# Kernel tuning notes

Measured on AMD Instinct MI355X. Metric: run time of the kernel, lower is better.

The kernel has to match this reference:

```python
import jax, jax.numpy as jnp
import numpy as np


def setup_inputs() -> dict:
    key = jax.random.key(0)
    k1, k2, k3, k4, k5 = jax.random.split(key, 5)
    b, c, k, h, w = 8, 512, 19, 128, 128
    x = jax.random.normal(k1, (b, c, h, w), dtype=jnp.float32)
    # mask_conv: 1x1 conv ichn->ochn (weight [k, c], bias [k])
    Wm = jax.random.normal(k2, (k, c), dtype=jnp.float32) * (1.0 / np.sqrt(c))
    bm = jax.random.normal(k3, (k,), dtype=jnp.float32) * 0.02
    # filter_conv: grouped 1x1 conv, groups=k -> per-class [c_out, c_in] matmul
    Wf = jax.random.normal(k4, (k, c, c), dtype=jnp.float32) * (1.0 / np.sqrt(c))
    bf = jax.random.normal(k5, (k, c), dtype=jnp.float32) * 0.02
    return {"x": x, "Wm": Wm, "bm": bm, "Wf": Wf, "bf": bf}


def reference(x, Wm, bm, Wf, bf):
    b, c, h, w = x.shape
    k = Wm.shape[0]
    # mask_conv (1x1) + sigmoid -> [b, k, h, w]
    pre_mask = jnp.einsum('bchw,kc->bkhw', x, Wm) + bm[None, :, None, None]
    mask = jax.nn.sigmoid(pre_mask)
    # masked pooling: bmm(mask [b,k,hw], feat [b,hw,c]) / (h*w) -> [b, k, c]
    class_feat = jnp.einsum('bkhw,bchw->bkc', mask, x) / (h * w)
    # grouped 1x1 filter_conv: per class k, [c_out, c_in] GEMM on class_feat
    filters = jnp.einsum('koc,bkc->bko', Wf, class_feat) + bf[None, :, :]  # [b, k, c]
    # per-sample dynamic 1x1 conv (groups=b) == batched GEMM over channels
    pred = jnp.einsum('bkc,bchw->bkhw', filters, x)
    return pred
```

## Files before the change

### kernel.cpp

```cpp
#include <hip/hip_runtime.h>
#include <math.h>

#define BB 8
#define CC 512
#define KK 19
#define HWHW 16384
#define INV_HW (1.0f/16384.0f)

typedef __attribute__((ext_vector_type(8))) short bf16x8;
typedef __attribute__((ext_vector_type(4))) short s16x4;
typedef __attribute__((ext_vector_type(4))) float f32x4;

__device__ __forceinline__ unsigned short f2bf(float f) {
    unsigned int u = __float_as_uint(f);
    u = (u + 0x7fffu + ((u >> 16) & 1u)) >> 16;
    return (unsigned short)u;
}

__device__ __forceinline__ unsigned int pk_bf16(float a, float b) {
    unsigned int r;
    asm("v_cvt_pk_bf16_f32 %0, %1, %2" : "=v"(r) : "v"(a), "v"(b));
    return r;
}

__global__ __launch_bounds__(256, 3) void k_s1(const float* __restrict__ x,
                                               const float* __restrict__ Wm,
                                               const float* __restrict__ bm,
                                               unsigned short* __restrict__ mask,
                                               unsigned short* __restrict__ xt4g,
                                               unsigned short* __restrict__ xt2g) {
    __shared__ short wm[20 * CC];
    __shared__ short xt[2][128 * 64];
    const int tid = threadIdx.x;
    const int b = blockIdx.x >> 7;
    const int pt = blockIdx.x & 127;
    const int p0 = pt << 7;
    const float* xb = x + ((size_t)b * CC) * HWHW + p0;

    for (int u = tid; u < 20 * 128; u += 256) {
        const int k = u >> 7;
        const int c4 = (u & 127) << 2;
        float4 w = {0.f, 0.f, 0.f, 0.f};
        if (k < KK) w = *(const float4*)(Wm + k * CC + c4);
        s16x4 v = { (short)f2bf(w.x), (short)f2bf(w.y), (short)f2bf(w.z), (short)f2bf(w.w) };
        *(s16x4*)&wm[(k << 9) + (((c4 >> 3) ^ (k & 7)) << 3) + (c4 & 7)] = v;
    }

    const int wv = tid >> 6, ln = tid & 63;
    const int lm = ln & 15, q = ln >> 4;
    const f32x4 zz = {0.f, 0.f, 0.f, 0.f};
    f32x4 acc[2][2];
    acc[0][0] = zz; acc[0][1] = zz; acc[1][0] = zz; acc[1][1] = zz;

    const int cg0 = tid >> 5;
    const int pA  = (tid & 31) << 2;
    const int pqT = (tid & 31) & 15;
    const int sS  = pt >> 3;
    const int kpT = ((pt & 7) << 1) | ((tid & 31) >> 4);
    const float* sA = xb + (size_t)(cg0 << 2) * HWHW + pA;
    const float* sB = xb + (size_t)((cg0 + 8) << 2) * HWHW + pA;
    unsigned short* t4fix = xt4g + ((size_t)((b << 7) | pt) << 16);
    unsigned short* t2fix = xt2g + ((size_t)(b << 3) << 20)
                                 + ((size_t)((sS << 4) | kpT) << 12);

    float4 Fa[8], Fb[8];
#pragma unroll
    for (int j = 0; j < 4; ++j) {
        Fa[j]     = *(const float4*)(sA + (size_t)j * HWHW);
        Fa[4 + j] = *(const float4*)(sB + (size_t)j * HWHW);
    }

#pragma unroll
    for (int cs = 0; cs < 8; ++cs) {
        const float4* cur = (cs & 1) ? Fb : Fa;
        float4* nxt = (cs & 1) ? Fa : Fb;
        if (cs < 7) {
            const size_t co = (size_t)((cs + 1) << 6) * HWHW;
#pragma unroll
            for (int j = 0; j < 4; ++j) {
                nxt[j]     = *(const float4*)(sA + co + (size_t)j * HWHW);
                nxt[4 + j] = *(const float4*)(sB + co + (size_t)j * HWHW);
            }
        }
        short* xts = (short*)xt[cs & 1];
        unsigned short* t4 = t4fix + ((size_t)cs << 13);
        unsigned short* t2 = t2fix + ((size_t)cs << 20);
#pragma unroll
        for (int h = 0; h < 2; ++h) {
            const int cg = cg0 + (h << 3);
            const float* G0 = (const float*)&cur[(h << 2) + 0];
            const float* G1 = (const float*)&cur[(h << 2) + 1];
            const float* G2 = (const float*)&cur[(h << 2) + 2];
            const float* G3 = (const float*)&cur[(h << 2) + 3];
#pragma unroll
            for (int j = 0; j < 4; ++j) {
                const int pr = pA + j;
                uint2 v = make_uint2(pk_bf16(G0[j], G1[j]), pk_bf16(G2[j], G3[j]));
                const int idx = (pr << 6) + (((cg >> 1) ^ (pr & 7)) << 3) + ((cg & 1) << 2);
                *(uint2*)&xts[idx] = v;
                *(uint2*)&t4[idx] = v;
            }
#pragma unroll
            for (int rr = 0; rr < 4; ++rr) {
                const int cl = (cg << 2) + rr;
                const float* Gr = (const float*)&cur[(h << 2) + rr];
                uint2 w = make_uint2(pk_bf16(Gr[0], Gr[1]), pk_bf16(Gr[2], Gr[3]));
                const int idx2 = (cl << 6) + (((pqT >> 1) ^ (cl & 7)) << 3) + ((pqT & 1) << 2);
                *(uint2*)&t2[idx2] = w;
            }
        }
        asm volatile("s_waitcnt lgkmcnt(0)" ::: "memory");
        __builtin_amdgcn_s_barrier();
        asm volatile("" ::: "memory");
#pragma unroll
        for (int ks = 0; ks < 2; ++ks) {
            const int gch = (cs << 3) + (ks << 2) + q;
            const int m1 = (lm < 3) ? (16 + lm) : 19;
            bf16x8 a0 = *(const bf16x8*)&wm[(lm << 9) + ((gch ^ (lm & 7)) << 3)];
            bf16x8 a1 = *(const bf16x8*)&wm[(m1 << 9) + ((gch ^ (m1 & 7)) << 3)];
            const int lch = (ks << 2) + q;
#pragma unroll
            for (int nt = 0; nt < 2; ++nt) {
                const int pr = (((wv << 1) + nt) << 4) + lm;
                bf16x8 bv = *(const bf16x8*)&xts[(pr << 6) + ((lch ^ (pr & 7)) << 3)];
                acc[0][nt] = __builtin_amdgcn_mfma_f32_16x16x32_bf16(a0, bv, acc[0][nt], 0, 0, 0);
                acc[1][nt] = __builtin_amdgcn_mfma_f32_16x16x32_bf16(a1, bv, acc[1][nt], 0, 0, 0);
            }
        }
    }

    unsigned short* mb = mask + ((size_t)b * KK) * HWHW + p0;
#pragma unroll
    for (int mt = 0; mt < 2; ++mt)
#pragma unroll
        for (int r = 0; r < 4; ++r) {
            const int k = (mt << 4) + (q << 2) + r;
            if (k < KK) {
                const float bias = bm[k];
#pragma unroll
                for (int nt = 0; nt < 2; ++nt) {
                    const int p = (((wv << 1) + nt) << 4) + lm;
                    const float t = acc[mt][nt][r] + bias;
                    mb[(size_t)k * HWHW + p] = f2bf(1.0f / (1.0f + __expf(-t)));
                }
            }
        }
}

__global__ __launch_bounds__(256, 4) void k_s2(const unsigned short* __restrict__ xt2g,
                                               const unsigned short* __restrict__ mask,
                                               float* __restrict__ cf_part) {
    __shared__ short mt_[2][20 * 64];
    __shared__ short xtl[2][64 * 64];
    const int tid = threadIdx.x;
    const int s = blockIdx.x & 15;
    const int ct = (blockIdx.x >> 4) & 7;
    const int b = blockIdx.x >> 7;
    const int wv = tid >> 6, ln = tid & 63;
    const int lm = ln & 15, q = ln >> 4;
    const unsigned short* mbs = mask + ((size_t)b * KK) * HWHW + (s << 10);
    const unsigned short* tb = xt2g + ((size_t)((((b << 3) | ct) << 4) | s) << 16);

    const int mk = tid >> 3, mch = tid & 7;

    const f32x4 zz = {0.f, 0.f, 0.f, 0.f};
    f32x4 acc[2];
    acc[0] = zz; acc[1] = zz;

    uint4 Xa[2], Xb2[2];
    uint4 Ma = make_uint4(0u,0u,0u,0u), Mb = make_uint4(0u,0u,0u,0u);

    if (tid < 160 && mk < KK) Ma = *(const uint4*)(mbs + (size_t)mk * HWHW + (mch << 3));
    Xa[0] = *(const uint4*)(tb + (tid << 4));
    Xa[1] = *(const uint4*)(tb + (tid << 4) + 8);

#pragma unroll
    for (int kp = 0; kp < 16; ++kp) {
        const uint4* curX = (kp & 1) ? Xb2 : Xa;
        uint4* nxtX = (kp & 1) ? Xa : Xb2;
        const uint4 curM = (kp & 1) ? Mb : Ma;
        uint4* nxtM = (kp & 1) ? &Ma : &Mb;
        if (kp < 15) {
            if (tid < 160 && mk < KK)
                *nxtM = *(const uint4*)(mbs + (size_t)mk * HWHW + ((kp + 1) << 6) + (mch << 3));
            nxtX[0] = *(const uint4*)(tb + ((kp + 1) << 12) + (tid << 4));
            nxtX[1] = *(const uint4*)(tb + ((kp + 1) << 12) + (tid << 4) + 8);
        }
        short* mts = (short*)mt_[kp & 1];
        short* xls = (short*)xtl[kp & 1];
        if (tid < 160)
            *(uint4*)&mts[(mk << 6) + ((mch ^ (mk & 7)) << 3)] = curM;
        *(uint4*)&xls[(tid << 4)] = curX[0];
        *(uint4*)&xls[(tid << 4) + 8] = curX[1];
        asm volatile("s_waitcnt lgkmcnt(0)" ::: "memory");
        __builtin_amdgcn_s_barrier();
        asm volatile("" ::: "memory");
#pragma unroll
        for (int ks = 0; ks < 2; ++ks) {
            const int pch = (ks << 2) + q;
            const int cr = (wv << 4) + lm;
            bf16x8 bv = *(const bf16x8*)&xls[(cr << 6) + ((pch ^ (cr & 7)) << 3)];
            const int m1 = (lm < 3) ? (16 + lm) : 19;
            bf16x8 a0 = *(const bf16x8*)&mts[(lm << 6) + ((pch ^ (lm & 7)) << 3)];
            bf16x8 a1 = *(const bf16x8*)&mts[(m1 << 6) + ((pch ^ (m1 & 7)) << 3)];
            acc[0] = __builtin_amdgcn_mfma_f32_16x16x32_bf16(a0, bv, acc[0], 0, 0, 0);
            acc[1] = __builtin_amdgcn_mfma_f32_16x16x32_bf16(a1, bv, acc[1], 0, 0, 0);
        }
    }

    float* dst = cf_part + ((size_t)(s * BB + b) * KK) * CC + (ct << 6) + (wv << 4) + lm;
#pragma unroll
    for (int mt = 0; mt < 2; ++mt)
#pragma unroll
        for (int r = 0; r < 4; ++r) {
            const int k = (mt << 4) + (q << 2) + r;
            if (k < KK) dst[(size_t)k * CC] = acc[mt][r];
        }
}

__global__ __launch_bounds__(256) void k_s2r(const float* __restrict__ part,
                                             float* __restrict__ cf) {
    const int i = blockIdx.x * 256 + threadIdx.x;
    if (i >= BB * KK * CC) return;
    const int b = i / (KK * CC);
    const int rem = i - b * (KK * CC);
    float sum = 0.0f;
#pragma unroll
    for (int s = 0; s < 16; ++s)
        sum += part[((size_t)(s * BB + b) * KK) * CC + rem];
    cf[i] = sum * INV_HW;
}

__global__ __launch_bounds__(256) void k_filters(const float* __restrict__ Wf,
                                                 const float* __restrict__ bf,
                                                 const float* __restrict__ cf,
                                                 float* __restrict__ fil) {
    const int blk = blockIdx.x;
    const int k = blk >> 7;
    const int o = ((blk & 127) << 2) + (threadIdx.x >> 6);
    const int lane = threadIdx.x & 63;
    const float* wrow = Wf + ((size_t)k * CC + o) * CC;

    float acc[BB];
#pragma unroll
    for (int b = 0; b < BB; ++b) acc[b] = 0.0f;
#pragma unroll
    for (int j = 0; j < CC / 64; ++j) {
        const int c = lane + (j << 6);
        const float wv = wrow[c];
#pragma unroll
        for (int b = 0; b < BB; ++b)
            acc[b] += wv * cf[((size_t)b * KK + k) * CC + c];
    }
#pragma unroll
    for (int b = 0; b < BB; ++b) {
#pragma unroll
        for (int off = 32; off > 0; off >>= 1)
            acc[b] += __shfl_down(acc[b], off, 64);
    }
    if (lane == 0) {
        const float bias = bf[k * CC + o];
#pragma unroll
        for (int b = 0; b < BB; ++b)
            fil[((size_t)b * KK + k) * CC + o] = acc[b] + bias;
    }
}

__global__ __launch_bounds__(256, 3) void k_s4(const unsigned short* __restrict__ xt4g,
                                               const float* __restrict__ fil,
                                               float* __restrict__ out) {
    __shared__ short wm[20 * CC];
    __shared__ short xt[2][128 * 64];
    const int tid = threadIdx.x;
    const int b = blockIdx.x >> 7;
    const int pt = blockIdx.x & 127;
    const int p0 = pt << 7;
    const float* fb = fil + ((size_t)b * KK) * CC;
    const unsigned short* tb = xt4g + ((size_t)((b << 7) | pt) << 16);

    for (int u = tid; u < 20 * 128; u += 256) {
        const int k = u >> 7;
        const int c4 = (u & 127) << 2;
        float4 w = {0.f, 0.f, 0.f, 0.f};
        if (k < KK) w = *(const float4*)(fb + k * CC + c4);
        s16x4 v = { (short)f2bf(w.x), (short)f2bf(w.y), (short)f2bf(w.z), (short)f2bf(w.w) };
        *(s16x4*)&wm[(k << 9) + (((c4 >> 3) ^ (k & 7)) << 3) + (c4 & 7)] = v;
    }

    const int wv = tid >> 6, ln = tid & 63;
    const int lm = ln & 15, q = ln >> 4;
    const f32x4 zz = {0.f, 0.f, 0.f, 0.f};
    f32x4 acc[2][2];
    acc[0][0] = zz; acc[0][1] = zz; acc[1][0] = zz; acc[1][1] = zz;

    uint4 Ta[4], Tb4[4];
#pragma unroll
    for (int r = 0; r < 4; ++r)
        Ta[r] = *(const uint4*)(tb + (tid << 5) + (r << 3));

#pragma unroll
    for (int cs = 0; cs < 8; ++cs) {
        const uint4* cur = (cs & 1) ? Tb4 : Ta;
        uint4* nxt = (cs & 1) ? Ta : Tb4;
        if (cs < 7) {
#pragma unroll
            for (int r = 0; r < 4; ++r)
                nxt[r] = *(const uint4*)(tb + ((cs + 1) << 13) + (tid << 5) + (r << 3));
        }
        short* xts = (short*)xt[cs & 1];
#pragma unroll
        for (int r = 0; r < 4; ++r)
            *(uint4*)&xts[(tid << 5) + (r << 3)] = cur[r];
        asm volatile("s_waitcnt lgkmcnt(0)" ::: "memory");
        __builtin_amdgcn_s_barrier();
        asm volatile("" ::: "memory");
#pragma unroll
        for (int ks = 0; ks < 2; ++ks) {
            const int gch = (cs << 3) + (ks << 2) + q;
            const int m1 = (lm < 3) ? (16 + lm) : 19;
            bf16x8 a0 = *(const bf16x8*)&wm[(lm << 9) + ((gch ^ (lm & 7)) << 3)];
            bf16x8 a1 = *(const bf16x8*)&wm[(m1 << 9) + ((gch ^ (m1 & 7)) << 3)];
            const int lch = (ks << 2) + q;
#pragma unroll
            for (int nt = 0; nt < 2; ++nt) {
                const int pr = (((wv << 1) + nt) << 4) + lm;
                bf16x8 bv = *(const bf16x8*)&xts[(pr << 6) + ((lch ^ (pr & 7)) << 3)];
                acc[0][nt] = __builtin_amdgcn_mfma_f32_16x16x32_bf16(a0, bv, acc[0][nt], 0, 0, 0);
                acc[1][nt] = __builtin_amdgcn_mfma_f32_16x16x32_bf16(a1, bv, acc[1][nt], 0, 0, 0);
            }
        }
    }

    float* ob = out + ((size_t)b * KK) * HWHW + p0;
#pragma unroll
    for (int mt = 0; mt < 2; ++mt)
#pragma unroll
        for (int r = 0; r < 4; ++r) {
            const int k = (mt << 4) + (q << 2) + r;
            if (k < KK) {
#pragma unroll
                for (int nt = 0; nt < 2; ++nt) {
                    const int p = (((wv << 1) + nt) << 4) + lm;
                    ob[(size_t)k * HWHW + p] = acc[mt][nt][r];
                }
            }
        }
}

extern "C" void kernel_launch(void* const* d_in, const int* in_sizes, int n_in,
                              void* d_out, int out_size, void* d_ws, size_t ws_size,
                              hipStream_t stream) {
    const float* x  = (const float*)d_in[0];
    const float* Wm = (const float*)d_in[1];
    const float* bm = (const float*)d_in[2];
    const float* Wf = (const float*)d_in[3];
    const float* bf = (const float*)d_in[4];
    float* out = (float*)d_out;

    char* p = (char*)d_ws;
    unsigned short* mask = (unsigned short*)p;  p += (size_t)BB * KK * HWHW * 2;
    float* cf_part = (float*)p;                 p += (size_t)16 * BB * KK * CC * 4;
    float* cf  = (float*)p;                     p += (size_t)BB * KK * CC * 4;
    float* fil = (float*)p;                     p += (size_t)BB * KK * CC * 4;
    unsigned short* xt4g = (unsigned short*)p;  p += (size_t)BB * 128 * 8 * 16384;
    unsigned short* xt2g = (unsigned short*)p;

    k_s1<<<1024, 256, 0, stream>>>(x, Wm, bm, mask, xt4g, xt2g);
    k_s2<<<1024, 256, 0, stream>>>(xt2g, mask, cf_part);
    k_s2r<<<(BB * KK * CC + 255) / 256, 256, 0, stream>>>(cf_part, cf);
    k_filters<<<KK * 128, 256, 0, stream>>>(Wf, bf, cf, fil);
    k_s4<<<1024, 256, 0, stream>>>(xt4g, fil, out);
}
```

Measured before the change: 505.6 us.

## Drop second transposed bf16 copy of x; share one layout for pooling and output

```diff
diff --git a/kernel.cpp b/kernel.cpp
--- a/kernel.cpp
+++ b/kernel.cpp
@@ -27,8 +27,7 @@
                                                const float* __restrict__ Wm,
                                                const float* __restrict__ bm,
                                                unsigned short* __restrict__ mask,
-                                               unsigned short* __restrict__ xt4g,
-                                               unsigned short* __restrict__ xt2g) {
+                                               unsigned short* __restrict__ xt4g) {
     __shared__ short wm[20 * CC];
     __shared__ short xt[2][128 * 64];
     const int tid = threadIdx.x;
@@ -54,14 +53,9 @@
 
     const int cg0 = tid >> 5;
     const int pA  = (tid & 31) << 2;
-    const int pqT = (tid & 31) & 15;
-    const int sS  = pt >> 3;
-    const int kpT = ((pt & 7) << 1) | ((tid & 31) >> 4);
     const float* sA = xb + (size_t)(cg0 << 2) * HWHW + pA;
     const float* sB = xb + (size_t)((cg0 + 8) << 2) * HWHW + pA;
     unsigned short* t4fix = xt4g + ((size_t)((b << 7) | pt) << 16);
-    unsigned short* t2fix = xt2g + ((size_t)(b << 3) << 20)
-                                 + ((size_t)((sS << 4) | kpT) << 12);
 
     float4 Fa[8], Fb[8];
 #pragma unroll
@@ -83,8 +77,6 @@
             }
         }
         short* xts = (short*)xt[cs & 1];
-        unsigned short* t4 = t4fix + ((size_t)cs << 13);
-        unsigned short* t2 = t2fix + ((size_t)cs << 20);
 #pragma unroll
         for (int h = 0; h < 2; ++h) {
             const int cg = cg0 + (h << 3);
@@ -98,15 +90,6 @@
                 uint2 v = make_uint2(pk_bf16(G0[j], G1[j]), pk_bf16(G2[j], G3[j]));
                 const int idx = (pr << 6) + (((cg >> 1) ^ (pr & 7)) << 3) + ((cg & 1) << 2);
                 *(uint2*)&xts[idx] = v;
-                *(uint2*)&t4[idx] = v;
-            }
-#pragma unroll
-            for (int rr = 0; rr < 4; ++rr) {
-                const int cl = (cg << 2) + rr;
-                const float* Gr = (const float*)&cur[(h << 2) + rr];
-                uint2 w = make_uint2(pk_bf16(Gr[0], Gr[1]), pk_bf16(Gr[2], Gr[3]));
-                const int idx2 = (cl << 6) + (((pqT >> 1) ^ (cl & 7)) << 3) + ((pqT & 1) << 2);
-                *(uint2*)&t2[idx2] = w;
             }
         }
         asm volatile("s_waitcnt lgkmcnt(0)" ::: "memory");
@@ -127,6 +110,14 @@
                 acc[1][nt] = __builtin_amdgcn_mfma_f32_16x16x32_bf16(a1, bv, acc[1][nt], 0, 0, 0);
             }
         }
+        {
+            unsigned short* t4 = t4fix + ((size_t)cs << 13);
+#pragma unroll
+            for (int r = 0; r < 4; ++r) {
+                uint4 v = *(const uint4*)&xts[(r << 11) + (tid << 3)];
+                *(uint4*)(t4 + (r << 11) + (tid << 3)) = v;
+            }
+        }
     }
 
     unsigned short* mb = mask + ((size_t)b * KK) * HWHW + p0;
@@ -147,68 +138,81 @@
         }
 }
 
-__global__ __launch_bounds__(256, 4) void k_s2(const unsigned short* __restrict__ xt2g,
+__global__ __launch_bounds__(256, 3) void k_s2(const unsigned short* __restrict__ xt4g,
                                                const unsigned short* __restrict__ mask,
                                                float* __restrict__ cf_part) {
-    __shared__ short mt_[2][20 * 64];
-    __shared__ short xtl[2][64 * 64];
+    __shared__ short xls[2][8192];
+    __shared__ short mtl[2][20 * 128];
     const int tid = threadIdx.x;
-    const int s = blockIdx.x & 15;
-    const int ct = (blockIdx.x >> 4) & 7;
+    const int cs = blockIdx.x & 7;
+    const int ptg = (blockIdx.x >> 3) & 15;
     const int b = blockIdx.x >> 7;
     const int wv = tid >> 6, ln = tid & 63;
     const int lm = ln & 15, q = ln >> 4;
-    const unsigned short* mbs = mask + ((size_t)b * KK) * HWHW + (s << 10);
-    const unsigned short* tb = xt2g + ((size_t)((((b << 3) | ct) << 4) | s) << 16);
-
-    const int mk = tid >> 3, mch = tid & 7;
+
+    const unsigned short* mb = mask + ((size_t)b * KK) * HWHW + (ptg << 10);
+    const unsigned short* tbase = xt4g + (((size_t)(((b << 4) | ptg) << 6) + cs) << 13);
+
+    const int mu1 = tid + 256;
+    const int k0 = tid >> 4, ch0 = tid & 15;
+    const int k1 = mu1 >> 4, ch1 = mu1 & 15;
 
     const f32x4 zz = {0.f, 0.f, 0.f, 0.f};
     f32x4 acc[2];
     acc[0] = zz; acc[1] = zz;
 
-    uint4 Xa[2], Xb2[2];
-    uint4 Ma = make_uint4(0u,0u,0u,0u), Mb = make_uint4(0u,0u,0u,0u);
-
-    if (tid < 160 && mk < KK) Ma = *(const uint4*)(mbs + (size_t)mk * HWHW + (mch << 3));
-    Xa[0] = *(const uint4*)(tb + (tid << 4));
-    Xa[1] = *(const uint4*)(tb + (tid << 4) + 8);
-
-#pragma unroll
-    for (int kp = 0; kp < 16; ++kp) {
-        const uint4* curX = (kp & 1) ? Xb2 : Xa;
-        uint4* nxtX = (kp & 1) ? Xa : Xb2;
-        const uint4 curM = (kp & 1) ? Mb : Ma;
-        uint4* nxtM = (kp & 1) ? &Ma : &Mb;
-        if (kp < 15) {
-            if (tid < 160 && mk < KK)
-                *nxtM = *(const uint4*)(mbs + (size_t)mk * HWHW + ((kp + 1) << 6) + (mch << 3));
-            nxtX[0] = *(const uint4*)(tb + ((kp + 1) << 12) + (tid << 4));
-            nxtX[1] = *(const uint4*)(tb + ((kp + 1) << 12) + (tid << 4) + 8);
-        }
-        short* mts = (short*)mt_[kp & 1];
-        short* xls = (short*)xtl[kp & 1];
-        if (tid < 160)
-            *(uint4*)&mts[(mk << 6) + ((mch ^ (mk & 7)) << 3)] = curM;
-        *(uint4*)&xls[(tid << 4)] = curX[0];
-        *(uint4*)&xls[(tid << 4) + 8] = curX[1];
+    uint4 Xa[4], Xb[4], Ma[2], Mb[2];
+    const uint4 z4 = make_uint4(0u, 0u, 0u, 0u);
+
+#pragma unroll
+    for (int r = 0; r < 4; ++r) Xa[r] = *(const uint4*)(tbase + (r << 11) + (tid << 3));
+    Ma[0] = z4; Ma[1] = z4;
+    if (k0 < KK) Ma[0] = *(const uint4*)(mb + (size_t)k0 * HWHW + (ch0 << 3));
+    if (mu1 < 320 && k1 < KK) Ma[1] = *(const uint4*)(mb + (size_t)k1 * HWHW + (ch1 << 3));
+
+#pragma unroll
+    for (int t = 0; t < 8; ++t) {
+        const uint4* curX = (t & 1) ? Xb : Xa;
+        uint4* nxtX = (t & 1) ? Xa : Xb;
+        const uint4* curM = (t & 1) ? Mb : Ma;
+        uint4* nxtM = (t & 1) ? Ma : Mb;
+        if (t < 7) {
+            const unsigned short* tp = tbase + ((size_t)(t + 1) << 16);
+#pragma unroll
+            for (int r = 0; r < 4; ++r) nxtX[r] = *(const uint4*)(tp + (r << 11) + (tid << 3));
+            nxtM[0] = z4; nxtM[1] = z4;
+            if (k0 < KK) nxtM[0] = *(const uint4*)(mb + (size_t)k0 * HWHW + ((t + 1) << 7) + (ch0 << 3));
+            if (mu1 < 320 && k1 < KK) nxtM[1] = *(const uint4*)(mb + (size_t)k1 * HWHW + ((t + 1) << 7) + (ch1 << 3));
+        }
+        short* xl = (short*)xls[t & 1];
+        short* ml = (short*)mtl[t & 1];
+#pragma unroll
+        for (int r = 0; r < 4; ++r) *(uint4*)&xl[(r << 11) + (tid << 3)] = curX[r];
+        *(uint4*)&ml[(k0 << 7) + ((ch0 ^ (k0 & 7)) << 3)] = curM[0];
+        if (mu1 < 320)
+            *(uint4*)&ml[(k1 << 7) + ((ch1 ^ (k1 & 7)) << 3)] = curM[1];
         asm volatile("s_waitcnt lgkmcnt(0)" ::: "memory");
         __builtin_amdgcn_s_barrier();
         asm volatile("" ::: "memory");
-#pragma unroll
-        for (int ks = 0; ks < 2; ++ks) {
-            const int pch = (ks << 2) + q;
-            const int cr = (wv << 4) + lm;
-            bf16x8 bv = *(const bf16x8*)&xls[(cr << 6) + ((pch ^ (cr & 7)) << 3)];
-            const int m1 = (lm < 3) ? (16 + lm) : 19;
-            bf16x8 a0 = *(const bf16x8*)&mts[(lm << 6) + ((pch ^ (lm & 7)) << 3)];
-            bf16x8 a1 = *(const bf16x8*)&mts[(m1 << 6) + ((pch ^ (m1 & 7)) << 3)];
+        const int c = (wv << 4) + lm;
+        const int m1 = (lm < 3) ? (16 + lm) : 19;
+#pragma unroll
+        for (int cc = 0; cc < 4; ++cc) {
+            const int pb = (cc << 5) + (q << 3);
+            short e[8];
+#pragma unroll
+            for (int i = 0; i < 8; ++i)
+                e[i] = xl[((pb + i) << 6) + (((c >> 3) ^ i) << 3) + (c & 7)];
+            bf16x8 bv = {e[0], e[1], e[2], e[3], e[4], e[5], e[6], e[7]};
+            const int pg = (cc << 2) + q;
+            bf16x8 a0 = *(const bf16x8*)&ml[(lm << 7) + ((pg ^ (lm & 7)) << 3)];
+            bf16x8 a1 = *(const bf16x8*)&ml[(m1 << 7) + ((pg ^ (m1 & 7)) << 3)];
             acc[0] = __builtin_amdgcn_mfma_f32_16x16x32_bf16(a0, bv, acc[0], 0, 0, 0);
             acc[1] = __builtin_amdgcn_mfma_f32_16x16x32_bf16(a1, bv, acc[1], 0, 0, 0);
         }
     }
 
-    float* dst = cf_part + ((size_t)(s * BB + b) * KK) * CC + (ct << 6) + (wv << 4) + lm;
+    float* dst = cf_part + ((size_t)(ptg * BB + b) * KK) * CC + (cs << 6) + (wv << 4) + lm;
 #pragma unroll
     for (int mt = 0; mt < 2; ++mt)
 #pragma unroll
@@ -296,7 +300,7 @@
     uint4 Ta[4], Tb4[4];
 #pragma unroll
     for (int r = 0; r < 4; ++r)
-        Ta[r] = *(const uint4*)(tb + (tid << 5) + (r << 3));
+        Ta[r] = *(const uint4*)(tb + (r << 11) + (tid << 3));
 
 #pragma unroll
     for (int cs = 0; cs < 8; ++cs) {
@@ -305,12 +309,12 @@
         if (cs < 7) {
 #pragma unroll
             for (int r = 0; r < 4; ++r)
-                nxt[r] = *(const uint4*)(tb + ((cs + 1) << 13) + (tid << 5) + (r << 3));
+                nxt[r] = *(const uint4*)(tb + ((size_t)(cs + 1) << 13) + (r << 11) + (tid << 3));
         }
         short* xts = (short*)xt[cs & 1];
 #pragma unroll
         for (int r = 0; r < 4; ++r)
-            *(uint4*)&xts[(tid << 5) + (r << 3)] = cur[r];
+            *(uint4*)&xts[(r << 11) + (tid << 3)] = cur[r];
         asm volatile("s_waitcnt lgkmcnt(0)" ::: "memory");
         __builtin_amdgcn_s_barrier();
         asm volatile("" ::: "memory");
@@ -362,11 +366,10 @@
     float* cf_part = (float*)p;                 p += (size_t)16 * BB * KK * CC * 4;
     float* cf  = (float*)p;                     p += (size_t)BB * KK * CC * 4;
     float* fil = (float*)p;                     p += (size_t)BB * KK * CC * 4;
-    unsigned short* xt4g = (unsigned short*)p;  p += (size_t)BB * 128 * 8 * 16384;
-    unsigned short* xt2g = (unsigned short*)p;
-
-    k_s1<<<1024, 256, 0, stream>>>(x, Wm, bm, mask, xt4g, xt2g);
-    k_s2<<<1024, 256, 0, stream>>>(xt2g, mask, cf_part);
+    unsigned short* xt4g = (unsigned short*)p;
+
+    k_s1<<<1024, 256, 0, stream>>>(x, Wm, bm, mask, xt4g);
+    k_s2<<<1024, 256, 0, stream>>>(xt4g, mask, cf_part);
     k_s2r<<<(BB * KK * CC + 255) / 256, 256, 0, stream>>>(cf_part, cf);
     k_filters<<<KK * 128, 256, 0, stream>>>(Wf, bf, cf, fil);
     k_s4<<<1024, 256, 0, stream>>>(xt4g, fil, out);
```

After: 460.2 us. 1.1x faster.
